# Kernel tuning notes

Measured on AMD Instinct MI355X. Metric: run time of the kernel, lower is better.

## Reference

```python
import jax, jax.numpy as jnp
import numpy as np

NEVENT = 1024
NSTEP = 64
NWINDOW = 2048
NHID = 128
NLAYER = 2


def _lstm_layer(x, Wih, Whh, bih, bhh):
    # x: [B, T, D]; PyTorch gate order: i, f, g, o
    B = x.shape[0]
    H = Whh.shape[1]
    h0 = jnp.zeros((B, H), x.dtype)
    c0 = jnp.zeros((B, H), x.dtype)
    b = bih + bhh

    def step(carry, xt):
        h, c = carry
        gates = xt @ Wih.T + h @ Whh.T + b  # [B, 4H]
        i, f, g, o = jnp.split(gates, 4, axis=-1)
        i = jax.nn.sigmoid(i)
        f = jax.nn.sigmoid(f)
        g = jnp.tanh(g)
        o = jax.nn.sigmoid(o)
        c = f * c + i * g
        h = o * jnp.tanh(c)
        return (h, c), h

    _, ys = jax.lax.scan(step, (h0, c0), jnp.swapaxes(x, 0, 1))  # ys: [T, B, H]
    return jnp.swapaxes(ys, 0, 1)


def _lstm(x, layers):
    for p in layers:
        x = _lstm_layer(x, *p)
    return x


def setup_inputs() -> dict:
    key = jax.random.key(0)
    ks = jax.random.split(key, 32)
    bound = 1.0 / np.sqrt(NHID)

    def u(k, shape):
        return jax.random.uniform(k, shape, jnp.float32, -bound, bound)

    inp = {"sequential": jax.random.randint(ks[0], (NWINDOW, NSTEP), 0, NEVENT)}
    i = 1
    for name, in0 in [("seq", 1), ("quant", NEVENT)]:
        for l in range(NLAYER):
            d = in0 if l == 0 else NHID
            inp[f"{name}_Wih{l}"] = u(ks[i], (4 * NHID, d)); i += 1
            inp[f"{name}_Whh{l}"] = u(ks[i], (4 * NHID, NHID)); i += 1
            inp[f"{name}_bih{l}"] = u(ks[i], (4 * NHID,)); i += 1
            inp[f"{name}_bhh{l}"] = u(ks[i], (4 * NHID,)); i += 1
    inp["cls_W"] = u(ks[i], (NEVENT, 2 * NHID)); i += 1
    inp["cls_b"] = u(ks[i], (NEVENT,))
    return inp


def reference(sequential,
              seq_Wih0, seq_Whh0, seq_bih0, seq_bhh0,
              seq_Wih1, seq_Whh1, seq_bih1, seq_bhh1,
              quant_Wih0, quant_Whh0, quant_bih0, quant_bhh0,
              quant_Wih1, quant_Whh1, quant_bih1, quant_bhh1,
              cls_W, cls_b):
    # sequential branch: embed (nemb=1 -> unsqueeze) then 2-layer LSTM
    seq_x = sequential[:, :, None].astype(jnp.float32)  # [B, T, 1]
    seq_out = _lstm(seq_x, [(seq_Wih0, seq_Whh0, seq_bih0, seq_bhh0),
                            (seq_Wih1, seq_Whh1, seq_bih1, seq_bhh1)])

    # quantitative branch: cumulative event-count histogram per window
    # (vectorized equivalent of the nested Counter loops): one-hot + cumsum over time
    quant = jnp.cumsum(jax.nn.one_hot(sequential, NEVENT, dtype=jnp.float32), axis=1)  # [B, T, E]
    quant_out = _lstm(quant, [(quant_Wih0, quant_Whh0, quant_bih0, quant_bhh0),
                              (quant_Wih1, quant_Whh1, quant_bih1, quant_bhh1)])

    out = jnp.concatenate([seq_out[:, -1], quant_out[:, -1]], axis=1)  # [B, 2H]
    return out @ cls_W.T + cls_b  # [B, nevent]
```

## Files before the change

### kernel.cpp

```cpp
#include <hip/hip_runtime.h>
#include <hip/hip_bf16.h>
#include <math.h>

#define NEVENT 1024
#define NSTEP 64
#define NWINDOW 2048
#define NHID 128
#define NG 512
#define WPB 8

typedef __attribute__((ext_vector_type(8))) short bf16x8;
typedef __attribute__((ext_vector_type(4))) float f32x4;

__device__ __forceinline__ unsigned short f2bf(float f){
  unsigned int u = __float_as_uint(f);
  return (unsigned short)((u + 0x7FFFu + ((u >> 16) & 1u)) >> 16);
}
__device__ __forceinline__ float sigm(float x){
  return __builtin_amdgcn_rcpf(1.0f + __expf(-x));
}
__device__ __forceinline__ float tanh_f(float x){
  float e = __expf(2.0f * x);
  return 1.0f - 2.0f * __builtin_amdgcn_rcpf(e + 1.0f);
}
__device__ __forceinline__ void lgkm_barrier(){
  asm volatile("s_waitcnt lgkmcnt(0)" ::: "memory");
  __builtin_amdgcn_s_barrier();
}
#define SWZ(row, byte) ((byte) ^ (((row) & 7) << 4))

__global__ __launch_bounds__(256)
void prep_k(const float* __restrict__ qWih0, float* __restrict__ qWqT,
            const float* __restrict__ clsW,  float* __restrict__ clsWT,
            const float* __restrict__ s0, const float* __restrict__ s1,
            const float* __restrict__ s2, const float* __restrict__ s3,
            const float* __restrict__ s4, const float* __restrict__ s5,
            unsigned short* __restrict__ dst)
{
  const int b = blockIdx.x;
  if (b < 768){
    const float* in; float* out; int R, C, bb;
    if (b < 512){ in = qWih0; out = qWqT; R = NG;     C = NEVENT; bb = b; }
    else        { in = clsW;  out = clsWT; R = NEVENT; C = 2*NHID; bb = b - 512; }
    __shared__ float tl[32][33];
    const int nbx = C >> 5;
    const int by = bb / nbx, bx = bb - by*nbx;
    const int tx = threadIdx.x & 31, ty = threadIdx.x >> 5;
    #pragma unroll
    for (int k = 0; k < 4; ++k){
      int r = by*32 + ty + k*8;
      tl[ty + k*8][tx] = in[r*C + bx*32 + tx];
    }
    __syncthreads();
    #pragma unroll
    for (int k = 0; k < 4; ++k){
      int r = bx*32 + ty + k*8;
      out[r*R + by*32 + tx] = tl[tx][ty + k*8];
    }
  } else {
    const int bb = b - 768;
    const int g = bb >> 5;
    const int i = (bb & 31)*256 + threadIdx.x;
    const float* src = (g==0)?s0:(g==1)?s1:(g==2)?s2:(g==3)?s3:(g==4)?s4:s5;
    unsigned short* d = dst + g*65536;
    const int lane = i & 63; const int n = (i >> 6) & 31; const int kt = i >> 11;
    const int col = 16*n + (lane & 15);
    const int k0  = 32*kt + 8*(lane >> 4);
    #pragma unroll
    for (int j = 0; j < 8; ++j)
      d[i*8 + j] = f2bf(src[col*128 + k0 + j]);
  }
}

__global__ __launch_bounds__(1024) __attribute__((amdgpu_waves_per_eu(4, 4)))
void lstm_fused_k(const int* __restrict__ seqtok,
    const float* __restrict__ sWih0,
    const float* __restrict__ sb0i, const float* __restrict__ sb0h,
    const float* __restrict__ sb1i, const float* __restrict__ sb1h,
    const float* __restrict__ qb0i, const float* __restrict__ qb0h,
    const float* __restrict__ qb1i, const float* __restrict__ qb1h,
    const unsigned short* __restrict__ pWhh0_s, const unsigned short* __restrict__ pWih1_s,
    const unsigned short* __restrict__ pWhh1_s,
    const unsigned short* __restrict__ pWhh0_q, const unsigned short* __restrict__ pWih1_q,
    const unsigned short* __restrict__ pWhh1_q,
    const float* __restrict__ qWqT,
    float* __restrict__ hseq, float* __restrict__ hq)
{
  __shared__ uint4 wih1[8192];
  __shared__ __attribute__((aligned(16))) unsigned short h0buf[2][2048];
  __shared__ __attribute__((aligned(16))) unsigned short h1buf[2][2048];
  __shared__ int sAll[16*64];

  const int tid  = threadIdx.x;
  const int lane = tid & 63;
  const int w    = tid >> 6;
  const bool quant = (blockIdx.x >= 128);
  const int blk  = quant ? (int)blockIdx.x - 128 : (int)blockIdx.x;
  const int w0   = blk * 16;

  const uint4* wsrc = (const uint4*)(quant ? pWih1_q : pWih1_s);
  for (int i = tid; i < 8192; i += 1024) wih1[i] = wsrc[i];
  sAll[tid] = seqtok[w0*64 + tid];
  for (int i = tid; i < 2048; i += 1024){ h0buf[0][i] = 0; h1buf[0][i] = 0; }

  const int rbase = 4*(lane >> 4);
  char* const h0base = (char*)h0buf;
  char* const h1base = (char*)h1buf;

  __syncthreads();

  if (w < 8){
    const int nw   = w;
    const int jcol = 16*nw + (lane & 15);
    const float* b1i = quant ? qb1i : sb1i; const float* b1h = quant ? qb1h : sb1h;
    float b1c[4];
    #pragma unroll
    for (int q = 0; q < 4; ++q){ int col = 128*q + jcol; b1c[q] = b1i[col] + b1h[col]; }
    const unsigned short* p1 = quant ? pWhh1_q : pWhh1_s;
    bf16x8 whh1f[4][4];
    #pragma unroll
    for (int q = 0; q < 4; ++q)
      #pragma unroll
      for (int kt = 0; kt < 4; ++kt)
        whh1f[q][kt] = *(const bf16x8*)(p1 + ((kt*32 + 8*q + nw)*64 + lane)*8);
    float c1[4] = {0,0,0,0};
    float* const houtp = quant ? hq : hseq;

    lgkm_barrier();

    for (int t = 0; t < NSTEP-1; ++t){
      char* h0rd = h0base + ((t+1)&1)*4096;
      char* h1rd = h1base + ((t  )&1)*4096;
      char* h1wr = h1base + ((t+1)&1)*4096;
      f32x4 acc[4];
      #pragma unroll
      for (int q = 0; q < 4; ++q){ f32x4 a; a[0]=b1c[q]; a[1]=b1c[q]; a[2]=b1c[q]; a[3]=b1c[q]; acc[q] = a; }
      #pragma unroll
      for (int kt = 0; kt < 4; ++kt){
        int row = lane & 15;
        int off = SWZ(row, row*256 + kt*64 + (lane>>4)*16);
        const bf16x8 a0 = *(const bf16x8*)(h0rd + off);
        const bf16x8 a1 = *(const bf16x8*)(h1rd + off);
        #pragma unroll
        for (int q = 0; q < 4; ++q){
          const bf16x8 wi = *(const bf16x8*)((const char*)wih1 + ((kt*32 + 8*q + nw)*64 + lane)*16);
          acc[q] = __builtin_amdgcn_mfma_f32_16x16x32_bf16(a0, wi,           acc[q], 0, 0, 0);
          acc[q] = __builtin_amdgcn_mfma_f32_16x16x32_bf16(a1, whh1f[q][kt], acc[q], 0, 0, 0);
        }
      }
      #pragma unroll
      for (int r = 0; r < 4; ++r){
        float iv = sigm(acc[0][r]), fv = sigm(acc[1][r]);
        float gv = tanh_f(acc[2][r]), ov = sigm(acc[3][r]);
        c1[r] = fv*c1[r] + iv*gv;
        float h = ov * tanh_f(c1[r]);
        int row = rbase + r;
        *(unsigned short*)(h1wr + SWZ(row, row*256 + jcol*2)) = f2bf(h);
      }
      lgkm_barrier();
    }

    {
      char* h0rd = h0base + 0*4096;
      char* h1rd = h1base + 1*4096;
      f32x4 acc[4];
      #pragma unroll
      for (int q = 0; q < 4; ++q){ f32x4 a; a[0]=b1c[q]; a[1]=b1c[q]; a[2]=b1c[q]; a[3]=b1c[q]; acc[q] = a; }
      #pragma unroll
      for (int kt = 0; kt < 4; ++kt){
        int row = lane & 15;
        int off = SWZ(row, row*256 + kt*64 + (lane>>4)*16);
        const bf16x8 a0 = *(const bf16x8*)(h0rd + off);
        const bf16x8 a1 = *(const bf16x8*)(h1rd + off);
        #pragma unroll
        for (int q = 0; q < 4; ++q){
          const bf16x8 wi = *(const bf16x8*)((const char*)wih1 + ((kt*32 + 8*q + nw)*64 + lane)*16);
          acc[q] = __builtin_amdgcn_mfma_f32_16x16x32_bf16(a0, wi,           acc[q], 0, 0, 0);
          acc[q] = __builtin_amdgcn_mfma_f32_16x16x32_bf16(a1, whh1f[q][kt], acc[q], 0, 0, 0);
        }
      }
      #pragma unroll
      for (int r = 0; r < 4; ++r){
        float iv = sigm(acc[0][r]), fv = sigm(acc[1][r]);
        float gv = tanh_f(acc[2][r]), ov = sigm(acc[3][r]);
        c1[r] = fv*c1[r] + iv*gv;
        float h = ov * tanh_f(c1[r]);
        int row = rbase + r;
        houtp[(w0 + row)*128 + jcol] = h;
      }
    }
  } else {
    const int nw   = w - 8;
    const int jcol = 16*nw + (lane & 15);
    const float* b0i = quant ? qb0i : sb0i; const float* b0h = quant ? qb0h : sb0h;
    float b0c[4];
    #pragma unroll
    for (int q = 0; q < 4; ++q){
      int col = 128*q + jcol;
      b0c[q] = b0i[col] + b0h[col];
    }
    const unsigned short* p0 = quant ? pWhh0_q : pWhh0_s;
    bf16x8 whh0f[4][4];
    #pragma unroll
    for (int q = 0; q < 4; ++q)
      #pragma unroll
      for (int kt = 0; kt < 4; ++kt)
        whh0f[q][kt] = *(const bf16x8*)(p0 + ((kt*32 + 8*q + nw)*64 + lane)*8);

    float c0[4] = {0,0,0,0};

    if (quant){
      float zr[4][4];
      #pragma unroll
      for (int q = 0; q < 4; ++q)
        #pragma unroll
        for (int r = 0; r < 4; ++r) zr[q][r] = b0c[q];
      {
        float gvv[4][4];
        #pragma unroll
        for (int r = 0; r < 4; ++r){
          int s = sAll[(rbase + r)*64 + 0];
          const float* gp = qWqT + s*512 + jcol;
          #pragma unroll
          for (int q = 0; q < 4; ++q) gvv[q][r] = gp[128*q];
        }
        float g0[4][4];
        #pragma unroll
        for (int q = 0; q < 4; ++q)
          #pragma unroll
          for (int r = 0; r < 4; ++r){ zr[q][r] += gvv[q][r]; g0[q][r] = zr[q][r]; }
        #pragma unroll
        for (int r = 0; r < 4; ++r){
          float iv = sigm(g0[0][r]);
          float gv = tanh_f(g0[2][r]);
          float ov = sigm(g0[3][r]);
          c0[r] = iv * gv;
          float h = ov * tanh_f(c0[r]);
          int row = rbase + r;
          *(unsigned short*)(h0base + 4096 + SWZ(row, row*256 + jcol*2)) = f2bf(h);
        }
      }
      lgkm_barrier();

      for (int t = 0; t < NSTEP-1; ++t){
        char* h0rd = h0base + ((t+1)&1)*4096;
        char* h0wr = h0base + ((t  )&1)*4096;
        float gvv[4][4];
        #pragma unroll
        for (int r = 0; r < 4; ++r){
          int s = sAll[(rbase + r)*64 + t + 1];
          const float* gp = qWqT + s*512 + jcol;
          #pragma unroll
          for (int q = 0; q < 4; ++q) gvv[q][r] = gp[128*q];
        }
        f32x4 acc[4];
        #pragma unroll
        for (int q = 0; q < 4; ++q){
          f32x4 a;
          #pragma unroll
          for (int r = 0; r < 4; ++r){ zr[q][r] += gvv[q][r]; a[r] = zr[q][r]; }
          acc[q] = a;
        }
        #pragma unroll
        for (int kt = 0; kt < 4; ++kt){
          int row = lane & 15;
          int off = SWZ(row, row*256 + kt*64 + (lane>>4)*16);
          const bf16x8 a0 = *(const bf16x8*)(h0rd + off);
          #pragma unroll
          for (int q = 0; q < 4; ++q)
            acc[q] = __builtin_amdgcn_mfma_f32_16x16x32_bf16(a0, whh0f[q][kt], acc[q], 0, 0, 0);
        }
        #pragma unroll
        for (int r = 0; r < 4; ++r){
          float iv = sigm(acc[0][r]), fv = sigm(acc[1][r]);
          float gv = tanh_f(acc[2][r]), ov = sigm(acc[3][r]);
          c0[r] = fv*c0[r] + iv*gv;
          float h = ov * tanh_f(c0[r]);
          int row = rbase + r;
          *(unsigned short*)(h0wr + SWZ(row, row*256 + jcol*2)) = f2bf(h);
        }
        lgkm_barrier();
      }
    } else {
      float wc[4];
      #pragma unroll
      for (int q = 0; q < 4; ++q) wc[q] = sWih0[128*q + jcol];
      {
        float g0[4][4];
        #pragma unroll
        for (int r = 0; r < 4; ++r){
          float sv = (float)sAll[(rbase + r)*64 + 0];
          #pragma unroll
          for (int q = 0; q < 4; ++q) g0[q][r] = fmaf(sv, wc[q], b0c[q]);
        }
        #pragma unroll
        for (int r = 0; r < 4; ++r){
          float iv = sigm(g0[0][r]);
          float gv = tanh_f(g0[2][r]);
          float ov = sigm(g0[3][r]);
          c0[r] = iv * gv;
          float h = ov * tanh_f(c0[r]);
          int row = rbase + r;
          *(unsigned short*)(h0base + 4096 + SWZ(row, row*256 + jcol*2)) = f2bf(h);
        }
      }
      lgkm_barrier();

      for (int t = 0; t < NSTEP-1; ++t){
        char* h0rd = h0base + ((t+1)&1)*4096;
        char* h0wr = h0base + ((t  )&1)*4096;
        f32x4 acc[4];
        float sv[4];
        #pragma unroll
        for (int r = 0; r < 4; ++r) sv[r] = (float)sAll[(rbase + r)*64 + t + 1];
        #pragma unroll
        for (int q = 0; q < 4; ++q){
          f32x4 a;
          #pragma unroll
          for (int r = 0; r < 4; ++r) a[r] = fmaf(sv[r], wc[q], b0c[q]);
          acc[q] = a;
        }
        #pragma unroll
        for (int kt = 0; kt < 4; ++kt){
          int row = lane & 15;
          int off = SWZ(row, row*256 + kt*64 + (lane>>4)*16);
          const bf16x8 a0 = *(const bf16x8*)(h0rd + off);
          #pragma unroll
          for (int q = 0; q < 4; ++q)
            acc[q] = __builtin_amdgcn_mfma_f32_16x16x32_bf16(a0, whh0f[q][kt], acc[q], 0, 0, 0);
        }
        #pragma unroll
        for (int r = 0; r < 4; ++r){
          float iv = sigm(acc[0][r]), fv = sigm(acc[1][r]);
          float gv = tanh_f(acc[2][r]), ov = sigm(acc[3][r]);
          c0[r] = fv*c0[r] + iv*gv;
          float h = ov * tanh_f(c0[r]);
          int row = rbase + r;
          *(unsigned short*)(h0wr + SWZ(row, row*256 + jcol*2)) = f2bf(h);
        }
        lgkm_barrier();
      }
    }
  }
}

__global__ __launch_bounds__(256, 4)
void cls_k(const float* __restrict__ hseq, const float* __restrict__ hq,
           const float* __restrict__ clsWT, const float* __restrict__ clsb,
           float* __restrict__ out)
{
  __shared__ float hcat[WPB][2*NHID];
  const int tid = threadIdx.x;
  const int w0 = blockIdx.x * WPB;
  for (int i = tid; i < WPB*2*NHID; i += 256){
    int w = i >> 8; int j = i & (2*NHID-1);
    hcat[w][j] = (j < NHID) ? hseq[(w0+w)*NHID + j] : hq[(w0+w)*NHID + (j - NHID)];
  }
  __syncthreads();
  float acc[4][WPB];
  #pragma unroll
  for (int p=0;p<4;++p)
    #pragma unroll
    for (int w=0;w<WPB;++w) acc[p][w] = 0.0f;
  for (int j = 0; j < 2*NHID; ++j){
    float wv0 = clsWT[j*NEVENT + tid];
    float wv1 = clsWT[j*NEVENT + tid + 256];
    float wv2 = clsWT[j*NEVENT + tid + 512];
    float wv3 = clsWT[j*NEVENT + tid + 768];
    #pragma unroll
    for (int w=0; w<WPB; ++w){
      float hv = hcat[w][j];
      acc[0][w] = fmaf(hv, wv0, acc[0][w]);
      acc[1][w] = fmaf(hv, wv1, acc[1][w]);
      acc[2][w] = fmaf(hv, wv2, acc[2][w]);
      acc[3][w] = fmaf(hv, wv3, acc[3][w]);
    }
  }
  #pragma unroll
  for (int p=0;p<4;++p){
    float bb = clsb[tid + p*256];
    #pragma unroll
    for (int w=0;w<WPB;++w)
      out[(w0+w)*NEVENT + tid + p*256] = acc[p][w] + bb;
  }
}

extern "C" void kernel_launch(void* const* d_in, const int* in_sizes, int n_in,
                              void* d_out, int out_size, void* d_ws, size_t ws_size,
                              hipStream_t stream) {
  const int*   seqtok = (const int*)  d_in[0];
  const float* sWih0  = (const float*)d_in[1];
  const float* sWhh0  = (const float*)d_in[2];
  const float* sb0i   = (const float*)d_in[3];
  const float* sb0h   = (const float*)d_in[4];
  const float* sWih1  = (const float*)d_in[5];
  const float* sWhh1  = (const float*)d_in[6];
  const float* sb1i   = (const float*)d_in[7];
  const float* sb1h   = (const float*)d_in[8];
  const float* qWih0  = (const float*)d_in[9];
  const float* qWhh0  = (const float*)d_in[10];
  const float* qb0i   = (const float*)d_in[11];
  const float* qb0h   = (const float*)d_in[12];
  const float* qWih1  = (const float*)d_in[13];
  const float* qWhh1  = (const float*)d_in[14];
  const float* qb1i   = (const float*)d_in[15];
  const float* qb1h   = (const float*)d_in[16];
  const float* clsW   = (const float*)d_in[17];
  const float* clsb   = (const float*)d_in[18];

  float* ws = (float*)d_ws;
  float* qWqT  = ws;
  float* clsWT = ws + 524288;
  float* hseq  = ws + 786432;
  float* hq    = ws + 1048576;
  unsigned short* pk = (unsigned short*)(ws + 1310720);
  unsigned short* pWhh0_s = pk;
  unsigned short* pWih1_s = pk + 65536;
  unsigned short* pWhh1_s = pk + 131072;
  unsigned short* pWhh0_q = pk + 196608;
  unsigned short* pWih1_q = pk + 262144;
  unsigned short* pWhh1_q = pk + 327680;

  prep_k<<<960, 256, 0, stream>>>(qWih0, qWqT, clsW, clsWT,
      sWhh0, sWih1, sWhh1, qWhh0, qWih1, qWhh1, pk);

  lstm_fused_k<<<256, 1024, 0, stream>>>(seqtok, sWih0,
      sb0i, sb0h, sb1i, sb1h, qb0i, qb0h, qb1i, qb1h,
      pWhh0_s, pWih1_s, pWhh1_s, pWhh0_q, pWih1_q, pWhh1_q,
      qWqT, hseq, hq);

  cls_k<<<NWINDOW/WPB, 256, 0, stream>>>(hseq, hq, clsWT, clsb, (float*)d_out);
}
```

Measured before the change: 211.0 us.

## Prefetch quant-layer gate gathers via async global-to-LDS loads overlapped with MFMA

In the quant layer-0 path, the per-step gather of transposed input-weight rows (indexed by token) is now issued as global_load_lds transfers into per-wave LDS slots. They are split into two halves that overlap the recurrent MFMA chain, and token ids are prefetched several steps ahead from global memory instead of the shared sAll table. The bias is also fed directly as the first MFMA accumulator. This aims to hide the latency of dependent gathered global loads on the serial recurrence, at the cost of manual vmcnt/lgkmcnt handling and extra LDS traffic.

```diff
diff --git a/kernel.cpp b/kernel.cpp
--- a/kernel.cpp
+++ b/kernel.cpp
@@ -26,6 +26,11 @@
 __device__ __forceinline__ void lgkm_barrier(){
   asm volatile("s_waitcnt lgkmcnt(0)" ::: "memory");
   __builtin_amdgcn_s_barrier();
+}
+__device__ __forceinline__ void gload4(const float* g, float* l){
+  __builtin_amdgcn_global_load_lds(
+      (const __attribute__((address_space(1))) void*)g,
+      (__attribute__((address_space(3))) void*)l, 4, 0, 0);
 }
 #define SWZ(row, byte) ((byte) ^ (((row) & 7) << 4))
 
@@ -89,7 +94,7 @@
   __shared__ uint4 wih1[8192];
   __shared__ __attribute__((aligned(16))) unsigned short h0buf[2][2048];
   __shared__ __attribute__((aligned(16))) unsigned short h1buf[2][2048];
-  __shared__ int sAll[16*64];
+  __shared__ float gbuf[8][8][64];
 
   const int tid  = threadIdx.x;
   const int lane = tid & 63;
@@ -100,7 +105,6 @@
 
   const uint4* wsrc = (const uint4*)(quant ? pWih1_q : pWih1_s);
   for (int i = tid; i < 8192; i += 1024) wih1[i] = wsrc[i];
-  sAll[tid] = seqtok[w0*64 + tid];
   for (int i = tid; i < 2048; i += 1024){ h0buf[0][i] = 0; h1buf[0][i] = 0; }
 
   const int rbase = 4*(lane >> 4);
@@ -113,9 +117,12 @@
     const int nw   = w;
     const int jcol = 16*nw + (lane & 15);
     const float* b1i = quant ? qb1i : sb1i; const float* b1h = quant ? qb1h : sb1h;
-    float b1c[4];
-    #pragma unroll
-    for (int q = 0; q < 4; ++q){ int col = 128*q + jcol; b1c[q] = b1i[col] + b1h[col]; }
+    f32x4 b1v[4];
+    #pragma unroll
+    for (int q = 0; q < 4; ++q){
+      int col = 128*q + jcol; float b = b1i[col] + b1h[col];
+      f32x4 v; v[0]=b; v[1]=b; v[2]=b; v[3]=b; b1v[q] = v;
+    }
     const unsigned short* p1 = quant ? pWhh1_q : pWhh1_s;
     bf16x8 whh1f[4][4];
     #pragma unroll
@@ -132,12 +139,21 @@
       char* h0rd = h0base + ((t+1)&1)*4096;
       char* h1rd = h1base + ((t  )&1)*4096;
       char* h1wr = h1base + ((t+1)&1)*4096;
+      const int row = lane & 15;
       f32x4 acc[4];
-      #pragma unroll
-      for (int q = 0; q < 4; ++q){ f32x4 a; a[0]=b1c[q]; a[1]=b1c[q]; a[2]=b1c[q]; a[3]=b1c[q]; acc[q] = a; }
-      #pragma unroll
-      for (int kt = 0; kt < 4; ++kt){
-        int row = lane & 15;
+      {
+        int off = SWZ(row, row*256 + 0*64 + (lane>>4)*16);
+        const bf16x8 a0 = *(const bf16x8*)(h0rd + off);
+        const bf16x8 a1 = *(const bf16x8*)(h1rd + off);
+        #pragma unroll
+        for (int q = 0; q < 4; ++q){
+          const bf16x8 wi = *(const bf16x8*)((const char*)wih1 + ((0*32 + 8*q + nw)*64 + lane)*16);
+          acc[q] = __builtin_amdgcn_mfma_f32_16x16x32_bf16(a0, wi,          b1v[q], 0, 0, 0);
+          acc[q] = __builtin_amdgcn_mfma_f32_16x16x32_bf16(a1, whh1f[q][0], acc[q], 0, 0, 0);
+        }
+      }
+      #pragma unroll
+      for (int kt = 1; kt < 4; ++kt){
         int off = SWZ(row, row*256 + kt*64 + (lane>>4)*16);
         const bf16x8 a0 = *(const bf16x8*)(h0rd + off);
         const bf16x8 a1 = *(const bf16x8*)(h1rd + off);
@@ -154,8 +170,8 @@
         float gv = tanh_f(acc[2][r]), ov = sigm(acc[3][r]);
         c1[r] = fv*c1[r] + iv*gv;
         float h = ov * tanh_f(c1[r]);
-        int row = rbase + r;
-        *(unsigned short*)(h1wr + SWZ(row, row*256 + jcol*2)) = f2bf(h);
+        int rw = rbase + r;
+        *(unsigned short*)(h1wr + SWZ(rw, rw*256 + jcol*2)) = f2bf(h);
       }
       lgkm_barrier();
     }
@@ -163,12 +179,21 @@
     {
       char* h0rd = h0base + 0*4096;
       char* h1rd = h1base + 1*4096;
+      const int row = lane & 15;
       f32x4 acc[4];
-      #pragma unroll
-      for (int q = 0; q < 4; ++q){ f32x4 a; a[0]=b1c[q]; a[1]=b1c[q]; a[2]=b1c[q]; a[3]=b1c[q]; acc[q] = a; }
-      #pragma unroll
-      for (int kt = 0; kt < 4; ++kt){
-        int row = lane & 15;
+      {
+        int off = SWZ(row, row*256 + 0*64 + (lane>>4)*16);
+        const bf16x8 a0 = *(const bf16x8*)(h0rd + off);
+        const bf16x8 a1 = *(const bf16x8*)(h1rd + off);
+        #pragma unroll
+        for (int q = 0; q < 4; ++q){
+          const bf16x8 wi = *(const bf16x8*)((const char*)wih1 + ((0*32 + 8*q + nw)*64 + lane)*16);
+          acc[q] = __builtin_amdgcn_mfma_f32_16x16x32_bf16(a0, wi,          b1v[q], 0, 0, 0);
+          acc[q] = __builtin_amdgcn_mfma_f32_16x16x32_bf16(a1, whh1f[q][0], acc[q], 0, 0, 0);
+        }
+      }
+      #pragma unroll
+      for (int kt = 1; kt < 4; ++kt){
         int off = SWZ(row, row*256 + kt*64 + (lane>>4)*16);
         const bf16x8 a0 = *(const bf16x8*)(h0rd + off);
         const bf16x8 a1 = *(const bf16x8*)(h1rd + off);
@@ -185,8 +210,8 @@
         float gv = tanh_f(acc[2][r]), ov = sigm(acc[3][r]);
         c1[r] = fv*c1[r] + iv*gv;
         float h = ov * tanh_f(c1[r]);
-        int row = rbase + r;
-        houtp[(w0 + row)*128 + jcol] = h;
+        int rw = rbase + r;
+        houtp[(w0 + rw)*128 + jcol] = h;
       }
     }
   } else {
@@ -208,27 +233,28 @@
         whh0f[q][kt] = *(const bf16x8*)(p0 + ((kt*32 + 8*q + nw)*64 + lane)*8);
 
     float c0[4] = {0,0,0,0};
+    const int* const tp = seqtok + (w0 + rbase)*64;
 
     if (quant){
-      float zr[4][4];
-      #pragma unroll
-      for (int q = 0; q < 4; ++q)
-        #pragma unroll
-        for (int r = 0; r < 4; ++r) zr[q][r] = b0c[q];
+      const float* const gq = qWqT + jcol;
+      float* const gslot = &gbuf[nw][0][0];
+      f32x4 zr[4];
+      #pragma unroll
+      for (int q = 0; q < 4; ++q){ f32x4 v; v[0]=b0c[q]; v[1]=b0c[q]; v[2]=b0c[q]; v[3]=b0c[q]; zr[q]=v; }
+
       {
-        float gvv[4][4];
-        #pragma unroll
-        for (int r = 0; r < 4; ++r){
-          int s = sAll[(rbase + r)*64 + 0];
-          const float* gp = qWqT + s*512 + jcol;
-          #pragma unroll
-          for (int q = 0; q < 4; ++q) gvv[q][r] = gp[128*q];
+        int u0 = tp[0], u1 = tp[64], u2 = tp[128], u3 = tp[192];
+        float pf[4][4];
+        #pragma unroll
+        for (int q = 0; q < 4; ++q){
+          pf[q][0] = gq[u0*512 + 128*q]; pf[q][1] = gq[u1*512 + 128*q];
+          pf[q][2] = gq[u2*512 + 128*q]; pf[q][3] = gq[u3*512 + 128*q];
         }
         float g0[4][4];
         #pragma unroll
         for (int q = 0; q < 4; ++q)
           #pragma unroll
-          for (int r = 0; r < 4; ++r){ zr[q][r] += gvv[q][r]; g0[q][r] = zr[q][r]; }
+          for (int r = 0; r < 4; ++r){ zr[q][r] += pf[q][r]; g0[q][r] = zr[q][r]; }
         #pragma unroll
         for (int r = 0; r < 4; ++r){
           float iv = sigm(g0[0][r]);
@@ -236,39 +262,86 @@
           float ov = sigm(g0[3][r]);
           c0[r] = iv * gv;
           float h = ov * tanh_f(c0[r]);
-          int row = rbase + r;
-          *(unsigned short*)(h0base + 4096 + SWZ(row, row*256 + jcol*2)) = f2bf(h);
-        }
-      }
+          int rw = rbase + r;
+          *(unsigned short*)(h0base + 4096 + SWZ(rw, rw*256 + jcol*2)) = f2bf(h);
+        }
+        int v0 = tp[1], v1 = tp[65], v2 = tp[129], v3 = tp[193];
+        #pragma unroll
+        for (int q = 0; q < 4; ++q){
+          pf[q][0] = gq[v0*512 + 128*q]; pf[q][1] = gq[v1*512 + 128*q];
+          pf[q][2] = gq[v2*512 + 128*q]; pf[q][3] = gq[v3*512 + 128*q];
+        }
+        #pragma unroll
+        for (int q = 0; q < 4; ++q)
+          #pragma unroll
+          for (int r = 0; r < 4; ++r) zr[q][r] += pf[q][r];
+      }
+      int tok0 = tp[2], tok1 = tp[66], tok2 = tp[130], tok3 = tp[194];
       lgkm_barrier();
 
       for (int t = 0; t < NSTEP-1; ++t){
         char* h0rd = h0base + ((t+1)&1)*4096;
         char* h0wr = h0base + ((t  )&1)*4096;
-        float gvv[4][4];
-        #pragma unroll
-        for (int r = 0; r < 4; ++r){
-          int s = sAll[(rbase + r)*64 + t + 1];
-          const float* gp = qWqT + s*512 + jcol;
-          #pragma unroll
-          for (int q = 0; q < 4; ++q) gvv[q][r] = gp[128*q];
-        }
+        const int row = lane & 15;
+        const float* ga0 = gq + tok0*512;
+        const float* ga1 = gq + tok1*512;
+        const float* ga2 = gq + tok2*512;
+        const float* ga3 = gq + tok3*512;
+        gload4(ga0,       gslot + 0*64);
+        gload4(ga1,       gslot + 1*64);
+        gload4(ga2,       gslot + 2*64);
+        gload4(ga3,       gslot + 3*64);
+        gload4(ga0 + 128, gslot + 4*64);
+        gload4(ga1 + 128, gslot + 5*64);
+        gload4(ga2 + 128, gslot + 6*64);
+        gload4(ga3 + 128, gslot + 7*64);
+        asm volatile("" ::: "memory");
+        int t3 = (t+3 < NSTEP) ? t+3 : NSTEP-1;
+        tok0 = tp[t3]; tok1 = tp[64+t3]; tok2 = tp[128+t3]; tok3 = tp[192+t3];
         f32x4 acc[4];
-        #pragma unroll
-        for (int q = 0; q < 4; ++q){
-          f32x4 a;
-          #pragma unroll
-          for (int r = 0; r < 4; ++r){ zr[q][r] += gvv[q][r]; a[r] = zr[q][r]; }
-          acc[q] = a;
-        }
-        #pragma unroll
-        for (int kt = 0; kt < 4; ++kt){
-          int row = lane & 15;
-          int off = SWZ(row, row*256 + kt*64 + (lane>>4)*16);
+        {
+          int off = SWZ(row, row*256 + 0*64 + (lane>>4)*16);
           const bf16x8 a0 = *(const bf16x8*)(h0rd + off);
           #pragma unroll
           for (int q = 0; q < 4; ++q)
-            acc[q] = __builtin_amdgcn_mfma_f32_16x16x32_bf16(a0, whh0f[q][kt], acc[q], 0, 0, 0);
+            acc[q] = __builtin_amdgcn_mfma_f32_16x16x32_bf16(a0, whh0f[q][0], zr[q], 0, 0, 0);
+        }
+        {
+          int off = SWZ(row, row*256 + 1*64 + (lane>>4)*16);
+          const bf16x8 a0 = *(const bf16x8*)(h0rd + off);
+          #pragma unroll
+          for (int q = 0; q < 4; ++q)
+            acc[q] = __builtin_amdgcn_mfma_f32_16x16x32_bf16(a0, whh0f[q][1], acc[q], 0, 0, 0);
+        }
+        asm volatile("s_waitcnt vmcnt(4)" ::: "memory");
+        {
+          float g0 = gslot[0*64+lane], g1 = gslot[1*64+lane], g2 = gslot[2*64+lane], g3 = gslot[3*64+lane];
+          float g4 = gslot[4*64+lane], g5 = gslot[5*64+lane], g6 = gslot[6*64+lane], g7 = gslot[7*64+lane];
+          zr[0][0] += g0; zr[0][1] += g1; zr[0][2] += g2; zr[0][3] += g3;
+          zr[1][0] += g4; zr[1][1] += g5; zr[1][2] += g6; zr[1][3] += g7;
+        }
+        asm volatile("s_waitcnt lgkmcnt(0)" ::: "memory");
+        gload4(ga0 + 256, gslot + 0*64);
+        gload4(ga1 + 256, gslot + 1*64);
+        gload4(ga2 + 256, gslot + 2*64);
+        gload4(ga3 + 256, gslot + 3*64);
+        gload4(ga0 + 384, gslot + 4*64);
+        gload4(ga1 + 384, gslot + 5*64);
+        gload4(ga2 + 384, gslot + 6*64);
+        gload4(ga3 + 384, gslot + 7*64);
+        {
+          int off = SWZ(row, row*256 + 2*64 + (lane>>4)*16);
+          const bf16x8 a0 = *(const bf16x8*)(h0rd + off);
+          #pragma unroll
+          for (int q = 0; q < 4; ++q)
+            acc[q] = __builtin_amdgcn_mfma_f32_16x16x32_bf16(a0, whh0f[q][2], acc[q], 0, 0, 0);
+        }
+        {
+          int off = SWZ(row, row*256 + 3*64 + (lane>>4)*16);
+          const bf16x8 a0 = *(const bf16x8*)(h0rd + off);
+          #pragma unroll
+          for (int q = 0; q < 4; ++q)
+            acc[q] = __builtin_amdgcn_mfma_f32_16x16x32_bf16(a0, whh0f[q][3], acc[q], 0, 0, 0);
         }
         #pragma unroll
         for (int r = 0; r < 4; ++r){
@@ -276,8 +349,15 @@
           float gv = tanh_f(acc[2][r]), ov = sigm(acc[3][r]);
           c0[r] = fv*c0[r] + iv*gv;
           float h = ov * tanh_f(c0[r]);
-          int row = rbase + r;
-          *(unsigned short*)(h0wr + SWZ(row, row*256 + jcol*2)) = f2bf(h);
+          int rw = rbase + r;
+          *(unsigned short*)(h0wr + SWZ(rw, rw*256 + jcol*2)) = f2bf(h);
+        }
+        asm volatile("s_waitcnt vmcnt(0)" ::: "memory");
+        {
+          float g0 = gslot[0*64+lane], g1 = gslot[1*64+lane], g2 = gslot[2*64+lane], g3 = gslot[3*64+lane];
+          float g4 = gslot[4*64+lane], g5 = gslot[5*64+lane], g6 = gslot[6*64+lane], g7 = gslot[7*64+lane];
+          zr[2][0] += g0; zr[2][1] += g1; zr[2][2] += g2; zr[2][3] += g3;
+          zr[3][0] += g4; zr[3][1] += g5; zr[3][2] += g6; zr[3][3] += g7;
         }
         lgkm_barrier();
       }
@@ -285,14 +365,15 @@
       float wc[4];
       #pragma unroll
       for (int q = 0; q < 4; ++q) wc[q] = sWih0[128*q + jcol];
+      int tok0, tok1, tok2, tok3;
       {
+        int u0 = tp[0], u1 = tp[64], u2 = tp[128], u3 = tp[192];
+        float sv[4] = {(float)u0, (float)u1, (float)u2, (float)u3};
         float g0[4][4];
         #pragma unroll
-        for (int r = 0; r < 4; ++r){
-          float sv = (float)sAll[(rbase + r)*64 + 0];
-          #pragma unroll
-          for (int q = 0; q < 4; ++q) g0[q][r] = fmaf(sv, wc[q], b0c[q]);
-        }
+        for (int r = 0; r < 4; ++r)
+          #pragma unroll
+          for (int q = 0; q < 4; ++q) g0[q][r] = fmaf(sv[r], wc[q], b0c[q]);
         #pragma unroll
         for (int r = 0; r < 4; ++r){
           float iv = sigm(g0[0][r]);
@@ -300,19 +381,21 @@
           float ov = sigm(g0[3][r]);
           c0[r] = iv * gv;
           float h = ov * tanh_f(c0[r]);
-          int row = rbase + r;
-          *(unsigned short*)(h0base + 4096 + SWZ(row, row*256 + jcol*2)) = f2bf(h);
-        }
+          int rw = rbase + r;
+          *(unsigned short*)(h0base + 4096 + SWZ(rw, rw*256 + jcol*2)) = f2bf(h);
+        }
+        tok0 = tp[1]; tok1 = tp[65]; tok2 = tp[129]; tok3 = tp[193];
       }
       lgkm_barrier();
 
       for (int t = 0; t < NSTEP-1; ++t){
         char* h0rd = h0base + ((t+1)&1)*4096;
         char* h0wr = h0base + ((t  )&1)*4096;
+        const int row = lane & 15;
+        float sv[4] = {(float)tok0, (float)tok1, (float)tok2, (float)tok3};
+        int t2 = (t+2 < NSTEP) ? t+2 : NSTEP-1;
+        tok0 = tp[t2]; tok1 = tp[64+t2]; tok2 = tp[128+t2]; tok3 = tp[192+t2];
         f32x4 acc[4];
-        float sv[4];
-        #pragma unroll
-        for (int r = 0; r < 4; ++r) sv[r] = (float)sAll[(rbase + r)*64 + t + 1];
         #pragma unroll
         for (int q = 0; q < 4; ++q){
           f32x4 a;
@@ -322,7 +405,6 @@
         }
         #pragma unroll
         for (int kt = 0; kt < 4; ++kt){
-          int row = lane & 15;
           int off = SWZ(row, row*256 + kt*64 + (lane>>4)*16);
           const bf16x8 a0 = *(const bf16x8*)(h0rd + off);
           #pragma unroll
@@ -335,8 +417,8 @@
           float gv = tanh_f(acc[2][r]), ov = sigm(acc[3][r]);
           c0[r] = fv*c0[r] + iv*gv;
           float h = ov * tanh_f(c0[r]);
-          int row = rbase + r;
-          *(unsigned short*)(h0wr + SWZ(row, row*256 + jcol*2)) = f2bf(h);
+          int rw = rbase + r;
+          *(unsigned short*)(h0wr + SWZ(rw, rw*256 + jcol*2)) = f2bf(h);
         }
         lgkm_barrier();
       }
```

New measurement: 237.6 us. 1.13x slower.
